# Optimization experiments

Hardware: AMD Instinct MI355X
Metric: run time of the kernel (lower is better)

Reference implementation:

```python
import jax, jax.numpy as jnp
import numpy as np

B, U, NBS, S = 128, 4, 64, 408
EM_WEIGHT = 0.01  # config['loss']['em_property_weight']


def setup_inputs() -> dict:
    key = jax.random.key(0)
    ks = jax.random.split(key, 11)
    return {
        "atten_re": jax.random.normal(ks[0], (B, U, S), jnp.float32),
        "atten_im": jax.random.normal(ks[1], (B, U, S), jnp.float32),
        "rad_re": jax.random.normal(ks[2], (B, U, NBS, S), jnp.float32),
        "rad_im": jax.random.normal(ks[3], (B, U, NBS, S), jnp.float32),
        "tgt_re": jax.random.normal(ks[4], (B, U, NBS, S), jnp.float32),
        "tgt_im": jax.random.normal(ks[5], (B, U, NBS, S), jnp.float32),
        "weights": jax.random.uniform(ks[6], (S,), jnp.float32),
        "positions": jax.random.normal(ks[7], (B, 3), jnp.float32),
        "ue_positions": jax.random.normal(ks[8], (B, 3), jnp.float32),
        "view_directions": jax.random.normal(ks[9], (B, 3), jnp.float32),
        "bs_antenna_ids": jax.random.randint(ks[10], (B,), 0, NBS, jnp.int64),
    }


def reference(atten_re, atten_im, rad_re, rad_im, tgt_re, tgt_im, weights,
              positions, ue_positions, view_directions, bs_antenna_ids):
    # Vectorized form of the triple loop: the ray-tracer stub contributes
    # nothing; accumulated signal = attenuation * radiation (complex mul),
    # with attenuation broadcast over the BS-antenna axis.
    ar = atten_re[:, :, None, :]  # [B,U,1,S]
    ai = atten_im[:, :, None, :]
    pred_re = ar * rad_re - ai * rad_im  # [B,U,NBS,S]
    pred_im = ar * rad_im + ai * rad_re
    # MSE on real + imag parts, weighted per subcarrier, summed.
    se = (pred_re - tgt_re) ** 2 + (pred_im - tgt_im) ** 2
    received_loss = jnp.sum(se * weights[None, None, None, :])
    # EM property regularization (torch.abs on complex -> magnitude).
    atten_mag = jnp.sqrt(atten_re ** 2 + atten_im ** 2)
    rad_mag = jnp.sqrt(rad_re ** 2 + rad_im ** 2)
    em_loss = (jnp.mean(jax.nn.relu(atten_mag - 1.0) ** 2)
               + jnp.mean(jax.nn.relu(rad_mag - 10.0) ** 2))
    return received_loss + EM_WEIGHT * em_loss
```

## Files before the change

### kernel.cpp

```cpp
#include <hip/hip_runtime.h>

constexpr int kB   = 128;
constexpr int kU   = 4;
constexpr int kNBS = 64;
constexpr int kS   = 408;
constexpr int kS4  = kS / 4;
constexpr unsigned kNQ = (unsigned)kB * kU * kNBS * kS4;
constexpr float kEmW     = 0.01f;
constexpr float kInvNRad = 1.0f / ((float)kB * kU * kNBS * kS);
constexpr float kInvNAtt = 1.0f / ((float)kB * kU * kS);

__global__ void __launch_bounds__(256)
prism_loss_kernel(const float4* __restrict__ atten_re,
                  const float4* __restrict__ atten_im,
                  const float4* __restrict__ rad_re,
                  const float4* __restrict__ rad_im,
                  const float4* __restrict__ tgt_re,
                  const float4* __restrict__ tgt_im,
                  const float4* __restrict__ weights,
                  float* __restrict__ out)
{
    float recv   = 0.0f;
    float em_rad = 0.0f;
    float em_att = 0.0f;

    const unsigned tid    = blockIdx.x * blockDim.x + threadIdx.x;
    const unsigned stride = gridDim.x * blockDim.x;

    for (unsigned q = tid; q < kNQ; q += stride) {
        const unsigned r    = q / (unsigned)kS4;
        const unsigned s4   = q - r * (unsigned)kS4;
        const unsigned arow = r >> 6;

        const float4 ar = atten_re[arow * kS4 + s4];
        const float4 ai = atten_im[arow * kS4 + s4];
        const float4 rr = rad_re[q];
        const float4 ri = rad_im[q];
        const float4 tr = tgt_re[q];
        const float4 ti = tgt_im[q];
        const float4 w  = weights[s4];

        const bool do_att = ((r & (kNBS - 1)) == 0);

#define PRISM_LANE(c)                                                        \
        {                                                                    \
            const float a_r = ar.c, a_i = ai.c;                              \
            const float r_r = rr.c, r_i = ri.c;                              \
            const float pr = a_r * r_r - a_i * r_i;                          \
            const float pi = a_r * r_i + a_i * r_r;                          \
            const float dr = pr - tr.c;                                      \
            const float di = pi - ti.c;                                      \
            recv = fmaf((dr * dr + di * di), w.c, recv);                     \
            float rm = sqrtf(fmaf(r_r, r_r, r_i * r_i)) - 10.0f;             \
            rm = fmaxf(rm, 0.0f);                                            \
            em_rad = fmaf(rm, rm, em_rad);                                   \
            if (do_att) {                                                    \
                float am = sqrtf(fmaf(a_r, a_r, a_i * a_i)) - 1.0f;          \
                am = fmaxf(am, 0.0f);                                        \
                em_att = fmaf(am, am, em_att);                               \
            }                                                                \
        }
        PRISM_LANE(x)
        PRISM_LANE(y)
        PRISM_LANE(z)
        PRISM_LANE(w)
#undef PRISM_LANE
    }

    float acc = recv + kEmW * (em_rad * kInvNRad + em_att * kInvNAtt);

    #pragma unroll
    for (int off = 32; off > 0; off >>= 1)
        acc += __shfl_down(acc, off, 64);

    __shared__ float sdata[4];
    const int lane = threadIdx.x & 63;
    const int wave = threadIdx.x >> 6;
    if (lane == 0) sdata[wave] = acc;
    __syncthreads();
    if (threadIdx.x == 0) {
        const float t = sdata[0] + sdata[1] + sdata[2] + sdata[3];
        atomicAdd(out, t);
    }
}

extern "C" void kernel_launch(void* const* d_in, const int* in_sizes, int n_in,
                              void* d_out, int out_size, void* d_ws, size_t ws_size,
                              hipStream_t stream) {
    const float4* atten_re = (const float4*)d_in[0];
    const float4* atten_im = (const float4*)d_in[1];
    const float4* rad_re   = (const float4*)d_in[2];
    const float4* rad_im   = (const float4*)d_in[3];
    const float4* tgt_re   = (const float4*)d_in[4];
    const float4* tgt_im   = (const float4*)d_in[5];
    const float4* weights  = (const float4*)d_in[6];
    float* out = (float*)d_out;

    hipMemsetAsync(out, 0, sizeof(float), stream);

    const int kBlocks = 3264;
    prism_loss_kernel<<<kBlocks, 256, 0, stream>>>(
        atten_re, atten_im, rad_re, rad_im, tgt_re, tgt_im, weights, out);
}
```

Baseline: 226.1 us.

## Replace grid-stride loop with fixed four-item per-thread batched loads

Each thread now handles exactly four float4 items spaced a quarter of the array apart and issues all 24 loads up front before computing. The per-iteration division and index math is done once, and the batched loads give more memory-level parallelism per thread. The grid becomes exactly sized to the problem, which raises register use and drops the generic loop, so the kernel only works for these fixed shapes.

```diff
diff --git a/kernel.cpp b/kernel.cpp
--- a/kernel.cpp
+++ b/kernel.cpp
@@ -6,6 +6,8 @@
 constexpr int kS   = 408;
 constexpr int kS4  = kS / 4;
 constexpr unsigned kNQ = (unsigned)kB * kU * kNBS * kS4;
+constexpr unsigned kThreads = kNQ / 4;
+constexpr unsigned kRowStep = 8192;
 constexpr float kEmW     = 0.01f;
 constexpr float kInvNRad = 1.0f / ((float)kB * kU * kNBS * kS);
 constexpr float kInvNAtt = 1.0f / ((float)kB * kU * kS);
@@ -20,36 +22,41 @@
                   const float4* __restrict__ weights,
                   float* __restrict__ out)
 {
+    const unsigned tid  = blockIdx.x * 256 + threadIdx.x;
+    const unsigned row0 = tid / 102u;
+    const unsigned s4   = tid - row0 * 102u;
+    const unsigned abase = (row0 >> 6) * 102u + s4;
+    const bool do_att = ((row0 & 63u) == 0u);
+
+    const float4 w = weights[s4];
+
+    float4 ar[4], ai[4], rr[4], ri[4], tr[4], ti[4];
+    #pragma unroll
+    for (int i = 0; i < 4; ++i) {
+        const unsigned q = tid + (unsigned)i * kThreads;
+        const unsigned a = abase + (unsigned)i * (kRowStep / kNBS) * 102u;
+        ar[i] = atten_re[a];
+        ai[i] = atten_im[a];
+        rr[i] = rad_re[q];
+        ri[i] = rad_im[q];
+        tr[i] = tgt_re[q];
+        ti[i] = tgt_im[q];
+    }
+
     float recv   = 0.0f;
     float em_rad = 0.0f;
     float em_att = 0.0f;
 
-    const unsigned tid    = blockIdx.x * blockDim.x + threadIdx.x;
-    const unsigned stride = gridDim.x * blockDim.x;
-
-    for (unsigned q = tid; q < kNQ; q += stride) {
-        const unsigned r    = q / (unsigned)kS4;
-        const unsigned s4   = q - r * (unsigned)kS4;
-        const unsigned arow = r >> 6;
-
-        const float4 ar = atten_re[arow * kS4 + s4];
-        const float4 ai = atten_im[arow * kS4 + s4];
-        const float4 rr = rad_re[q];
-        const float4 ri = rad_im[q];
-        const float4 tr = tgt_re[q];
-        const float4 ti = tgt_im[q];
-        const float4 w  = weights[s4];
-
-        const bool do_att = ((r & (kNBS - 1)) == 0);
-
+    #pragma unroll
+    for (int i = 0; i < 4; ++i) {
 #define PRISM_LANE(c)                                                        \
         {                                                                    \
-            const float a_r = ar.c, a_i = ai.c;                              \
-            const float r_r = rr.c, r_i = ri.c;                              \
+            const float a_r = ar[i].c, a_i = ai[i].c;                        \
+            const float r_r = rr[i].c, r_i = ri[i].c;                        \
             const float pr = a_r * r_r - a_i * r_i;                          \
             const float pi = a_r * r_i + a_i * r_r;                          \
-            const float dr = pr - tr.c;                                      \
-            const float di = pi - ti.c;                                      \
+            const float dr = pr - tr[i].c;                                   \
+            const float di = pi - ti[i].c;                                   \
             recv = fmaf((dr * dr + di * di), w.c, recv);                     \
             float rm = sqrtf(fmaf(r_r, r_r, r_i * r_i)) - 10.0f;             \
             rm = fmaxf(rm, 0.0f);                                            \
@@ -79,8 +86,7 @@
     if (lane == 0) sdata[wave] = acc;
     __syncthreads();
     if (threadIdx.x == 0) {
-        const float t = sdata[0] + sdata[1] + sdata[2] + sdata[3];
-        atomicAdd(out, t);
+        atomicAdd(out, sdata[0] + sdata[1] + sdata[2] + sdata[3]);
     }
 }
 
@@ -98,7 +104,6 @@
 
     hipMemsetAsync(out, 0, sizeof(float), stream);
 
-    const int kBlocks = 3264;
-    prism_loss_kernel<<<kBlocks, 256, 0, stream>>>(
+    prism_loss_kernel<<<(int)(kThreads / 256), 256, 0, stream>>>(
         atten_re, atten_im, rad_re, rad_im, tgt_re, tgt_im, weights, out);
 }
```

Result: no change. 224.1 us (-0.9%).
